# Kernel optimization log

Hardware: AMD Instinct MI355X
Metric: run time of the kernel (lower is better)

The kernel has to match this reference:

```python
import jax, jax.numpy as jnp
import numpy as np
from jax import lax

B, C_IN, C_OUT, H, W, K, MID = 16, 256, 256, 64, 64, 3, 64
BN_EPS = 1e-5


def setup_inputs() -> dict:
    key = jax.random.key(0)
    ks = jax.random.split(key, 16)
    inp = {
        'x': jax.random.normal(ks[0], (B, C_IN, H, W), dtype=jnp.float32),
        # 4 kernel banks: (4, c2, c1//g, k, k)
        'weight': jax.random.normal(ks[1], (4, C_OUT, C_IN, K, K), dtype=jnp.float32) * 0.05,
        'gamma': jnp.ones((C_OUT,), jnp.float32),
        'beta': jnp.zeros((C_OUT,), jnp.float32),
    }
    # four attention branches: Linear(c, mid, bias=False) -> ReLU -> Linear(mid, 4, bias=True)
    names = ['s', 'c', 'f', 'w']
    for i, n in enumerate(names):
        inp[f'fc_{n}_w1'] = jax.random.normal(ks[2 + 3 * i], (MID, C_IN), dtype=jnp.float32) * 0.05
        inp[f'fc_{n}_w2'] = jax.random.normal(ks[3 + 3 * i], (4, MID), dtype=jnp.float32) * 0.05
        inp[f'fc_{n}_b2'] = jax.random.normal(ks[4 + 3 * i], (4,), dtype=jnp.float32) * 0.05
    return inp


def _branch(pooled, w1, w2, b2):
    # pooled: [B, C]; w1: [MID, C]; w2: [4, MID]
    h = jax.nn.relu(pooled @ w1.T)
    return jax.nn.softmax(h @ w2.T + b2, axis=1)  # [B, 4]


def reference(x, weight, gamma, beta,
              fc_s_w1, fc_s_w2, fc_s_b2,
              fc_c_w1, fc_c_w2, fc_c_b2,
              fc_f_w1, fc_f_w2, fc_f_b2,
              fc_w_w1, fc_w_w2, fc_w_b2):
    b = x.shape[0]
    pooled = jnp.mean(x, axis=(2, 3))  # GAP -> [B, C]
    alpha = (_branch(pooled, fc_s_w1, fc_s_w2, fc_s_b2)
             * _branch(pooled, fc_c_w1, fc_c_w2, fc_c_b2)
             * _branch(pooled, fc_f_w1, fc_f_w2, fc_f_b2)
             * _branch(pooled, fc_w_w1, fc_w_w2, fc_w_b2))  # [B, 4]
    # per-sample dynamic kernels: [B, out_c, in_c, k, k]
    dyn_w = jnp.einsum('bn,noikl->boikl', alpha, weight)

    def conv_one(xi, wi):
        # xi: [C, H, W]; wi: [out_c, in_c, k, k]
        return lax.conv_general_dilated(
            xi[None], wi, window_strides=(1, 1), padding='SAME',
            dimension_numbers=('NCHW', 'OIHW', 'NCHW'))[0]

    out = jax.vmap(conv_one)(x, dyn_w)  # [B, out_c, H, W]

    # BatchNorm2d (training-mode batch statistics)
    mean = jnp.mean(out, axis=(0, 2, 3))
    var = jnp.var(out, axis=(0, 2, 3))
    out = (out - mean[None, :, None, None]) * jax.lax.rsqrt(var + BN_EPS)[None, :, None, None]
    return out * gamma[None, :, None, None] + beta[None, :, None, None]
```

## Files before the change

### kernel.cpp

```cpp
#include <hip/hip_runtime.h>
#include <math.h>

#define BB 16
#define CIN 256
#define COUT 256
#define HH 64
#define WW 64
#define NBANK_STRIDE 589824

typedef short bf16x8 __attribute__((ext_vector_type(8)));
typedef float f32x4 __attribute__((ext_vector_type(4)));

#define WS_XT_OFF 32768
#define WS_DW_OFF 33587200
#define WS_NEED   52461568ULL

static __device__ __forceinline__ short f2bf(float f) {
    union { float f; unsigned u; } v; v.f = f;
    unsigned r = v.u + 0x7FFF + ((v.u >> 16) & 1);
    return (short)(r >> 16);
}

struct AttnParams {
    const float* w1[4];
    const float* w2[4];
    const float* b2[4];
};

__global__ __launch_bounds__(256) void zero_kernel(float* __restrict__ ws) {
    ws[blockIdx.x * 256 + threadIdx.x] = 0.f;
}

__global__ __launch_bounds__(256) void xpose_kernel(const float* __restrict__ x,
                                                    short* __restrict__ xT,
                                                    float* __restrict__ pooled) {
    const int ci0 = blockIdx.x * 32;
    const int h = blockIdx.y;
    const int b = blockIdx.z;
    const int t = threadIdx.x;
    __shared__ __align__(16) short tile[64][40];
    {
        const int ci = t >> 3;
        const int l = t & 7;
        const float4* src = (const float4*)(x + ((size_t)(b * 256 + ci0 + ci)) * 4096 + h * 64);
        float4 v1 = src[l * 2];
        float4 v2 = src[l * 2 + 1];
        tile[l * 8 + 0][ci] = f2bf(v1.x);
        tile[l * 8 + 1][ci] = f2bf(v1.y);
        tile[l * 8 + 2][ci] = f2bf(v1.z);
        tile[l * 8 + 3][ci] = f2bf(v1.w);
        tile[l * 8 + 4][ci] = f2bf(v2.x);
        tile[l * 8 + 5][ci] = f2bf(v2.y);
        tile[l * 8 + 6][ci] = f2bf(v2.z);
        tile[l * 8 + 7][ci] = f2bf(v2.w);
        float s = v1.x + v1.y + v1.z + v1.w + v2.x + v2.y + v2.z + v2.w;
        s += __shfl_xor(s, 1, 64);
        s += __shfl_xor(s, 2, 64);
        s += __shfl_xor(s, 4, 64);
        if (l == 0) atomicAdd(&pooled[b * 256 + ci0 + ci], s);
    }
    __syncthreads();
    {
        const int w = t >> 2;
        const int s = t & 3;
        bf16x8 val = *(const bf16x8*)&tile[w][s * 8];
        *(bf16x8*)&xT[((size_t)b * 4096 + h * 64 + w) * 256 + ci0 + s * 8] = val;
    }
}

__global__ __launch_bounds__(256) void attn_kernel(AttnParams p, float* __restrict__ ws_f) {
    const int b = blockIdx.x;
    const int t = threadIdx.x;
    const int wv = t >> 6;
    const int lane = t & 63;
    __shared__ float ps[256];
    __shared__ float hs[4][64];
    __shared__ float lg[4][4];
    __shared__ float sm[4][4];
    ws_f[4096 + b * 256 + t] = 0.f;
    ps[t] = ws_f[b * 256 + t] * (1.0f / 4096.0f);
    __syncthreads();
    {
        const float4* w1v = (const float4*)(p.w1[wv] + lane * 256);
        float h = 0.f;
#pragma unroll 8
        for (int i = 0; i < 64; ++i) {
            float4 w4 = w1v[i];
            h += w4.x * ps[i * 4 + 0] + w4.y * ps[i * 4 + 1] +
                 w4.z * ps[i * 4 + 2] + w4.w * ps[i * 4 + 3];
        }
        hs[wv][lane] = fmaxf(h, 0.f);
    }
    __syncthreads();
    if (t < 16) {
        const int n = t >> 2, j = t & 3;
        const float* w2 = p.w2[n];
        float l = p.b2[n][j];
        for (int m = 0; m < 64; ++m) l += w2[j * 64 + m] * hs[n][m];
        lg[n][j] = l;
    }
    __syncthreads();
    if (t < 4) {
        const int n = t;
        float mx = fmaxf(fmaxf(lg[n][0], lg[n][1]), fmaxf(lg[n][2], lg[n][3]));
        float e0 = expf(lg[n][0] - mx), e1 = expf(lg[n][1] - mx);
        float e2 = expf(lg[n][2] - mx), e3 = expf(lg[n][3] - mx);
        float inv = 1.f / (e0 + e1 + e2 + e3);
        sm[n][0] = e0 * inv; sm[n][1] = e1 * inv; sm[n][2] = e2 * inv; sm[n][3] = e3 * inv;
    }
    __syncthreads();
    if (t < 4) ws_f[b * 256 + t] = sm[0][t] * sm[1][t] * sm[2][t] * sm[3][t];
}

__global__ __launch_bounds__(256) void dynw_kernel(const float* __restrict__ wt,
                                                   const float* __restrict__ ws_f,
                                                   short* __restrict__ dynwT) {
    const int co = blockIdx.x;
    const int ci = threadIdx.x;
    float w[4][9];
#pragma unroll
    for (int n = 0; n < 4; ++n) {
        const size_t base = ((size_t)(n * 256 + co) * 256 + ci) * 9;
#pragma unroll
        for (int k = 0; k < 9; ++k) w[n][k] = wt[base + k];
    }
    for (int b = 0; b < BB; ++b) {
        const float a0 = ws_f[b * 256 + 0];
        const float a1 = ws_f[b * 256 + 1];
        const float a2 = ws_f[b * 256 + 2];
        const float a3 = ws_f[b * 256 + 3];
#pragma unroll
        for (int k = 0; k < 9; ++k) {
            float v = a0 * w[0][k] + a1 * w[1][k] + a2 * w[2][k] + a3 * w[3][k];
            dynwT[((size_t)(b * 9 + k) * 256 + co) * 256 + ci] = f2bf(v);
        }
    }
}

__global__ __launch_bounds__(256, 2) void conv_mfma_kernel(const short* __restrict__ xT,
                                                           const short* __restrict__ dynwT,
                                                           float* __restrict__ out,
                                                           float* __restrict__ bn_part) {
    const int nt = blockIdx.x;
    const int mt = blockIdx.y;
    const int b = blockIdx.z;
    const int t = threadIdx.x;
    const int lane = t & 63;
    const int wv = t >> 6;
    const int wx = wv & 1;
    const int wy = wv >> 1;
    const int mh = lane & 15;
    const int q = lane >> 4;
    const int r0 = nt * 4;
    const int co0 = mt * 128;

    __shared__ __align__(16) short xs[396 * 40];
    __shared__ __align__(16) short As[2][128 * 40];
    __shared__ float red[128][2][2];

    f32x4 acc[4][8];
#pragma unroll
    for (int i = 0; i < 4; ++i)
#pragma unroll
        for (int j = 0; j < 8; ++j) acc[i][j] = (f32x4){0.f, 0.f, 0.f, 0.f};

    const int arow0 = t >> 2;
    const int asub = t & 3;
    const short* Ab = dynwT + (size_t)b * 9 * 65536 + (co0 + arow0) * 256 + asub * 8;
    const int a_lds0 = arow0 * 40 + asub * 8;
    const int a_lds1 = (arow0 + 64) * 40 + asub * 8;
    const int a_rd = (wy * 64 + mh) * 40 + q * 8;

    const bf16x8 zero8 = {0, 0, 0, 0, 0, 0, 0, 0};

    for (int cc = 0; cc < 8; ++cc) {
        const int ci0 = cc * 32;
        __syncthreads();
        bf16x8 pa0 = *(const bf16x8*)(Ab + ci0);
        bf16x8 pa1 = *(const bf16x8*)(Ab + 64 * 256 + ci0);
#pragma unroll
        for (int i = 0; i < 7; ++i) {
            int idx = t + 256 * i;
            if (idx < 1584) {
                int p = idx >> 2;
                int sub = idx & 3;
                int lr = p / 66;
                int lc = p - lr * 66;
                int r = r0 - 1 + lr;
                int c = lc - 1;
                bf16x8 v = zero8;
                if ((unsigned)r < 64u && (unsigned)c < 64u)
                    v = *(const bf16x8*)&xT[((size_t)b * 4096 + r * 64 + c) * 256 + ci0 + sub * 8];
                *(bf16x8*)&xs[p * 40 + sub * 8] = v;
            }
        }
        *(bf16x8*)&As[0][a_lds0] = pa0;
        *(bf16x8*)&As[0][a_lds1] = pa1;
        __syncthreads();
#pragma unroll
        for (int khw = 0; khw < 9; ++khw) {
            const int kh = khw / 3;
            const int kw = khw - kh * 3;
            bf16x8 na0, na1;
            if (khw < 8) {
                na0 = *(const bf16x8*)(Ab + (khw + 1) * 65536 + ci0);
                na1 = *(const bf16x8*)(Ab + (khw + 1) * 65536 + 64 * 256 + ci0);
            }
            bf16x8 bfr[8];
#pragma unroll
            for (int ni = 0; ni < 8; ++ni) {
                const int row_l = wx * 2 + (ni >> 2) + kh;
                const int col_l = (ni & 3) * 16 + kw + mh;
                bfr[ni] = *(const bf16x8*)&xs[(row_l * 66 + col_l) * 40 + q * 8];
            }
#pragma unroll
            for (int mi = 0; mi < 4; ++mi) {
                bf16x8 af = *(const bf16x8*)&As[khw & 1][a_rd + mi * 640];
#pragma unroll
                for (int ni = 0; ni < 8; ++ni)
                    acc[mi][ni] = __builtin_amdgcn_mfma_f32_16x16x32_bf16(af, bfr[ni], acc[mi][ni], 0, 0, 0);
            }
            if (khw < 8) {
                *(bf16x8*)&As[(khw + 1) & 1][a_lds0] = na0;
                *(bf16x8*)&As[(khw + 1) & 1][a_lds1] = na1;
            }
            __syncthreads();
        }
    }

    float s16[4][4], q16[4][4];
#pragma unroll
    for (int mi = 0; mi < 4; ++mi)
#pragma unroll
        for (int reg = 0; reg < 4; ++reg) { s16[mi][reg] = 0.f; q16[mi][reg] = 0.f; }

#pragma unroll
    for (int mi = 0; mi < 4; ++mi) {
#pragma unroll
        for (int ni = 0; ni < 8; ++ni) {
            const int pix = wx * 128 + ni * 16 + mh;
            const int h = r0 + (pix >> 6);
            const int w = pix & 63;
#pragma unroll
            for (int reg = 0; reg < 4; ++reg) {
                const int co = co0 + wy * 64 + mi * 16 + q * 4 + reg;
                const float e = acc[mi][ni][reg];
                out[(((size_t)b * 256 + co) << 12) + (h << 6) + w] = e;
                s16[mi][reg] += e;
                q16[mi][reg] += e * e;
            }
        }
    }
#pragma unroll
    for (int mi = 0; mi < 4; ++mi)
#pragma unroll
        for (int reg = 0; reg < 4; ++reg) {
            float s = s16[mi][reg], sq = q16[mi][reg];
            s += __shfl_xor(s, 1, 64);  sq += __shfl_xor(sq, 1, 64);
            s += __shfl_xor(s, 2, 64);  sq += __shfl_xor(sq, 2, 64);
            s += __shfl_xor(s, 4, 64);  sq += __shfl_xor(sq, 4, 64);
            s += __shfl_xor(s, 8, 64);  sq += __shfl_xor(sq, 8, 64);
            if (mh == 0) {
                const int co_l = wy * 64 + mi * 16 + q * 4 + reg;
                red[co_l][0][wx] = s;
                red[co_l][1][wx] = sq;
            }
        }
    __syncthreads();
    {
        const int co_l = t >> 1;
        const int st = t & 1;
        float v = red[co_l][st][0] + red[co_l][st][1];
        atomicAdd(&bn_part[(st * 256 + co0 + co_l) * 8 + (nt & 7)], v);
    }
}

__global__ __launch_bounds__(256) void bn_finalize_kernel(const float* __restrict__ bn_part,
                                                          const float* __restrict__ gamma,
                                                          const float* __restrict__ beta,
                                                          float* __restrict__ scale,
                                                          float* __restrict__ shift) {
    const int co = threadIdx.x;
    float S = 0.f, Q = 0.f;
#pragma unroll
    for (int s = 0; s < 8; ++s) {
        S += bn_part[(co) * 8 + s];
        Q += bn_part[(256 + co) * 8 + s];
    }
    const float mean = S * (1.f / 65536.f);
    const float var = Q * (1.f / 65536.f) - mean * mean;
    const float inv = rsqrtf(var + 1e-5f);
    const float sc = gamma[co] * inv;
    scale[co] = sc;
    shift[co] = beta[co] - mean * sc;
}

__global__ __launch_bounds__(256) void bn_apply_kernel(float* __restrict__ out,
                                                       const float* __restrict__ scale,
                                                       const float* __restrict__ shift) {
    const int gid = blockIdx.x * 256 + threadIdx.x;
    const int c = (gid >> 10) & 255;
    float4* p = (float4*)out;
    float4 v = p[gid];
    const float sc = scale[c], sh = shift[c];
    v.x = v.x * sc + sh;
    v.y = v.y * sc + sh;
    v.z = v.z * sc + sh;
    v.w = v.w * sc + sh;
    p[gid] = v;
}

__global__ __launch_bounds__(256) void gap_kernel(const float* __restrict__ x,
                                                  float* __restrict__ pooled) {
    const int plane = blockIdx.x;
    const float4* p = (const float4*)(x + (size_t)plane * 4096);
    const int t = threadIdx.x;
    float s = 0.f;
#pragma unroll
    for (int i = 0; i < 4; ++i) {
        float4 v = p[t + 256 * i];
        s += v.x + v.y + v.z + v.w;
    }
#pragma unroll
    for (int off = 32; off > 0; off >>= 1) s += __shfl_down(s, off, 64);
    __shared__ float red[4];
    if ((t & 63) == 0) red[t >> 6] = s;
    __syncthreads();
    if (t == 0) pooled[plane] = (red[0] + red[1] + red[2] + red[3]) * (1.0f / 4096.0f);
}

__global__ __launch_bounds__(64) void attn64_kernel(const float* __restrict__ pooled,
                                                    AttnParams p,
                                                    float* __restrict__ alpha) {
    const int b = blockIdx.x;
    const int t = threadIdx.x;
    __shared__ float ps[256];
    __shared__ float hs[64];
    __shared__ float lg[4];
    __shared__ float prod[4];
#pragma unroll
    for (int i = 0; i < 4; ++i) ps[t + 64 * i] = pooled[b * 256 + t + 64 * i];
    if (t < 4) prod[t] = 1.f;
    __syncthreads();
    for (int n = 0; n < 4; ++n) {
        const float* w1 = p.w1[n];
        float h = 0.f;
        for (int c = 0; c < 256; ++c) h += w1[t * 256 + c] * ps[c];
        hs[t] = fmaxf(h, 0.f);
        __syncthreads();
        if (t < 4) {
            const float* w2 = p.w2[n];
            float l = p.b2[n][t];
            for (int m = 0; m < 64; ++m) l += w2[t * 64 + m] * hs[m];
            lg[t] = l;
        }
        __syncthreads();
        if (t == 0) {
            float mx = fmaxf(fmaxf(lg[0], lg[1]), fmaxf(lg[2], lg[3]));
            float e0 = expf(lg[0] - mx), e1 = expf(lg[1] - mx);
            float e2 = expf(lg[2] - mx), e3 = expf(lg[3] - mx);
            float inv = 1.f / (e0 + e1 + e2 + e3);
            prod[0] *= e0 * inv; prod[1] *= e1 * inv;
            prod[2] *= e2 * inv; prod[3] *= e3 * inv;
        }
        __syncthreads();
    }
    if (t < 4) alpha[b * 4 + t] = prod[t];
}

__global__ __launch_bounds__(256) void conv_fp32_kernel(const float* __restrict__ x,
                                                        const float* __restrict__ wt,
                                                        const float* __restrict__ alpha,
                                                        float* __restrict__ out) {
    const int h = blockIdx.x;
    const int cot = blockIdx.y;
    const int b = blockIdx.z;
    const int t = threadIdx.x;
    const int tx = t & 15;
    const int ty = t >> 4;
    const int co0 = cot * 64;
    __shared__ __align__(16) float xsf[32][68];
    __shared__ __align__(16) float wshf[3][32][68];
    const float a0 = alpha[b * 4 + 0], a1 = alpha[b * 4 + 1];
    const float a2 = alpha[b * 4 + 2], a3 = alpha[b * 4 + 3];
    float acc[4][4];
#pragma unroll
    for (int i = 0; i < 4; ++i)
#pragma unroll
        for (int j = 0; j < 4; ++j) acc[i][j] = 0.f;
    const size_t xbase = (size_t)b * CIN * 4096;
    for (int kh = 0; kh < 3; ++kh) {
        const int r = h + kh - 1;
        if (r < 0 || r >= HH) continue;
        for (int chunk = 0; chunk < 8; ++chunk) {
            const int ci0 = chunk * 32;
            __syncthreads();
#pragma unroll
            for (int i = 0; i < 8; ++i) {
                int flat = t + 256 * i;
                int ci = flat >> 6;
                int w = flat & 63;
                xsf[ci][1 + w] = x[xbase + (size_t)(ci0 + ci) * 4096 + r * 64 + w];
            }
            if (t < 32) { xsf[t][0] = 0.f; xsf[t][65] = 0.f; xsf[t][66] = 0.f; xsf[t][67] = 0.f; }
#pragma unroll
            for (int j = 0; j < 24; ++j) {
                int e = t + 256 * j;
                int co = e / 96;
                int rem = e - co * 96;
                int ci = rem / 3;
                int kw = rem - ci * 3;
                size_t g = (((size_t)(co0 + co) * 256 + (ci0 + ci)) * 3 + kh) * 3 + kw;
                wshf[kw][ci][co] = a0 * wt[g] + a1 * wt[g + NBANK_STRIDE] +
                                   a2 * wt[g + 2 * NBANK_STRIDE] + a3 * wt[g + 3 * NBANK_STRIDE];
            }
            __syncthreads();
            for (int ci = 0; ci < 32; ++ci) {
                float4 w0 = *(const float4*)&wshf[0][ci][tx * 4];
                float4 w1v = *(const float4*)&wshf[1][ci][tx * 4];
                float4 w2v = *(const float4*)&wshf[2][ci][tx * 4];
                float4 xa = *(const float4*)&xsf[ci][ty * 4];
                float4 xb = *(const float4*)&xsf[ci][ty * 4 + 4];
                float v[8] = {xa.x, xa.y, xa.z, xa.w, xb.x, xb.y, xb.z, xb.w};
                float aw[3][4] = {{w0.x, w0.y, w0.z, w0.w},
                                  {w1v.x, w1v.y, w1v.z, w1v.w},
                                  {w2v.x, w2v.y, w2v.z, w2v.w}};
#pragma unroll
                for (int kw = 0; kw < 3; ++kw)
#pragma unroll
                    for (int i = 0; i < 4; ++i)
#pragma unroll
                        for (int j = 0; j < 4; ++j)
                            acc[i][j] += aw[kw][i] * v[j + kw];
            }
        }
    }
    size_t obase = (((size_t)b * COUT + co0 + tx * 4) * 64 + h) * 64 + ty * 4;
#pragma unroll
    for (int i = 0; i < 4; ++i) {
        float4 o = {acc[i][0], acc[i][1], acc[i][2], acc[i][3]};
        *(float4*)&out[obase + (size_t)i * 4096] = o;
    }
}

__global__ __launch_bounds__(256) void bn_stats_kernel(const float* __restrict__ out,
                                                       const float* __restrict__ gamma,
                                                       const float* __restrict__ beta,
                                                       float* __restrict__ scale,
                                                       float* __restrict__ shift) {
    const int co = blockIdx.x;
    const int t = threadIdx.x;
    float s = 0.f, sq = 0.f;
    for (int b = 0; b < BB; ++b) {
        const float4* p = (const float4*)(out + ((size_t)b * 256 + co) * 4096);
#pragma unroll
        for (int i = 0; i < 4; ++i) {
            float4 v = p[t + 256 * i];
            s += v.x + v.y + v.z + v.w;
            sq += v.x * v.x + v.y * v.y + v.z * v.z + v.w * v.w;
        }
    }
#pragma unroll
    for (int off = 32; off > 0; off >>= 1) {
        s += __shfl_down(s, off, 64);
        sq += __shfl_down(sq, off, 64);
    }
    __shared__ float rs[4], rq[4];
    if ((t & 63) == 0) { rs[t >> 6] = s; rq[t >> 6] = sq; }
    __syncthreads();
    if (t == 0) {
        float S = rs[0] + rs[1] + rs[2] + rs[3];
        float Q = rq[0] + rq[1] + rq[2] + rq[3];
        float mean = S * (1.f / 65536.f);
        float var = Q * (1.f / 65536.f) - mean * mean;
        float inv = rsqrtf(var + 1e-5f);
        float sc = gamma[co] * inv;
        scale[co] = sc;
        shift[co] = beta[co] - mean * sc;
    }
}

extern "C" void kernel_launch(void* const* d_in, const int* in_sizes, int n_in,
                              void* d_out, int out_size, void* d_ws, size_t ws_size,
                              hipStream_t stream) {
    (void)in_sizes; (void)n_in; (void)out_size;
    const float* x = (const float*)d_in[0];
    const float* wt = (const float*)d_in[1];
    const float* gamma = (const float*)d_in[2];
    const float* beta = (const float*)d_in[3];
    AttnParams ap;
    for (int n = 0; n < 4; ++n) {
        ap.w1[n] = (const float*)d_in[4 + 3 * n];
        ap.w2[n] = (const float*)d_in[5 + 3 * n];
        ap.b2[n] = (const float*)d_in[6 + 3 * n];
    }
    float* ws_f = (float*)d_ws;
    float* out = (float*)d_out;

    if (ws_size >= WS_NEED) {
        short* xT = (short*)((char*)d_ws + WS_XT_OFF);
        short* dynwT = (short*)((char*)d_ws + WS_DW_OFF);
        float* bn_part = ws_f + 4096;
        float* scale = ws_f;
        float* shift = ws_f + 256;

        zero_kernel<<<16, 256, 0, stream>>>(ws_f);
        xpose_kernel<<<dim3(8, 64, 16), 256, 0, stream>>>(x, xT, ws_f);
        attn_kernel<<<16, 256, 0, stream>>>(ap, ws_f);
        dynw_kernel<<<256, 256, 0, stream>>>(wt, ws_f, dynwT);
        conv_mfma_kernel<<<dim3(16, 2, 16), 256, 0, stream>>>(xT, dynwT, out, bn_part);
        bn_finalize_kernel<<<1, 256, 0, stream>>>(bn_part, gamma, beta, scale, shift);
        bn_apply_kernel<<<16384, 256, 0, stream>>>(out, scale, shift);
    } else {
        float* pooled = ws_f;
        float* alpha = ws_f + 4096;
        float* scale = ws_f + 4160;
        float* shift = ws_f + 4416;
        gap_kernel<<<4096, 256, 0, stream>>>(x, pooled);
        attn64_kernel<<<16, 64, 0, stream>>>(pooled, ap, alpha);
        conv_fp32_kernel<<<dim3(64, 4, 16), 256, 0, stream>>>(x, wt, alpha, out);
        bn_stats_kernel<<<256, 256, 0, stream>>>(out, gamma, beta, scale, shift);
        bn_apply_kernel<<<16384, 256, 0, stream>>>(out, scale, shift);
    }
}
```

Before: 277.8 us.

## Load conv weight fragments directly to registers, fold BN finalize into apply, stage dynw via LDS

The conv kernel no longer stages the dynamic-weight A tile in shared memory. Each lane loads its MFMA A fragments straight from global memory into registers, prefetched one k-step ahead across channel chunks, which removes the per-khw __syncthreads and LDS writes and reads. The BN finalize kernel is merged into the apply kernel, so each block recomputes its channel's scale and shift, saving one launch. dynw_kernel now loads the weights coalesced into LDS before the per-thread gather. The trade-off is more global-memory traffic for the A operand, since each wave loads its own fragments, plus higher register pressure.

```diff
diff --git a/kernel.cpp b/kernel.cpp
--- a/kernel.cpp
+++ b/kernel.cpp
@@ -116,14 +116,21 @@
                                                    const float* __restrict__ ws_f,
                                                    short* __restrict__ dynwT) {
     const int co = blockIdx.x;
-    const int ci = threadIdx.x;
+    const int t = threadIdx.x;
+    __shared__ float wl[4][2304];
+#pragma unroll
+    for (int n = 0; n < 4; ++n) {
+        const float* src = wt + ((size_t)(n * 256 + co)) * 2304;
+#pragma unroll
+        for (int i = 0; i < 9; ++i) wl[n][t + 256 * i] = src[t + 256 * i];
+    }
+    __syncthreads();
+    const int ci = t;
     float w[4][9];
 #pragma unroll
-    for (int n = 0; n < 4; ++n) {
-        const size_t base = ((size_t)(n * 256 + co) * 256 + ci) * 9;
-#pragma unroll
-        for (int k = 0; k < 9; ++k) w[n][k] = wt[base + k];
-    }
+    for (int n = 0; n < 4; ++n)
+#pragma unroll
+        for (int k = 0; k < 9; ++k) w[n][k] = wl[n][ci * 9 + k];
     for (int b = 0; b < BB; ++b) {
         const float a0 = ws_f[b * 256 + 0];
         const float a1 = ws_f[b * 256 + 1];
@@ -155,7 +162,6 @@
     const int co0 = mt * 128;
 
     __shared__ __align__(16) short xs[396 * 40];
-    __shared__ __align__(16) short As[2][128 * 40];
     __shared__ float red[128][2][2];
 
     f32x4 acc[4][8];
@@ -164,20 +170,17 @@
 #pragma unroll
         for (int j = 0; j < 8; ++j) acc[i][j] = (f32x4){0.f, 0.f, 0.f, 0.f};
 
-    const int arow0 = t >> 2;
-    const int asub = t & 3;
-    const short* Ab = dynwT + (size_t)b * 9 * 65536 + (co0 + arow0) * 256 + asub * 8;
-    const int a_lds0 = arow0 * 40 + asub * 8;
-    const int a_lds1 = (arow0 + 64) * 40 + asub * 8;
-    const int a_rd = (wy * 64 + mh) * 40 + q * 8;
+    const short* Abase = dynwT + (size_t)b * 9 * 65536 + (size_t)(co0 + wy * 64 + mh) * 256 + q * 8;
+
+    bf16x8 ca[4], na[4];
+#pragma unroll
+    for (int mi = 0; mi < 4; ++mi) ca[mi] = *(const bf16x8*)(Abase + mi * 4096);
 
     const bf16x8 zero8 = {0, 0, 0, 0, 0, 0, 0, 0};
 
     for (int cc = 0; cc < 8; ++cc) {
         const int ci0 = cc * 32;
         __syncthreads();
-        bf16x8 pa0 = *(const bf16x8*)(Ab + ci0);
-        bf16x8 pa1 = *(const bf16x8*)(Ab + 64 * 256 + ci0);
 #pragma unroll
         for (int i = 0; i < 7; ++i) {
             int idx = t + 256 * i;
@@ -194,18 +197,18 @@
                 *(bf16x8*)&xs[p * 40 + sub * 8] = v;
             }
         }
-        *(bf16x8*)&As[0][a_lds0] = pa0;
-        *(bf16x8*)&As[0][a_lds1] = pa1;
         __syncthreads();
 #pragma unroll
         for (int khw = 0; khw < 9; ++khw) {
+            const int kk = cc * 9 + khw;
+            const int nk = (kk < 71) ? kk + 1 : 71;
+            const int nkhw = nk - (nk / 9) * 9;
+            const int nci0 = (nk / 9) * 32;
+#pragma unroll
+            for (int mi = 0; mi < 4; ++mi)
+                na[mi] = *(const bf16x8*)(Abase + (size_t)nkhw * 65536 + mi * 4096 + nci0);
             const int kh = khw / 3;
             const int kw = khw - kh * 3;
-            bf16x8 na0, na1;
-            if (khw < 8) {
-                na0 = *(const bf16x8*)(Ab + (khw + 1) * 65536 + ci0);
-                na1 = *(const bf16x8*)(Ab + (khw + 1) * 65536 + 64 * 256 + ci0);
-            }
             bf16x8 bfr[8];
 #pragma unroll
             for (int ni = 0; ni < 8; ++ni) {
@@ -214,17 +217,12 @@
                 bfr[ni] = *(const bf16x8*)&xs[(row_l * 66 + col_l) * 40 + q * 8];
             }
 #pragma unroll
-            for (int mi = 0; mi < 4; ++mi) {
-                bf16x8 af = *(const bf16x8*)&As[khw & 1][a_rd + mi * 640];
+            for (int mi = 0; mi < 4; ++mi)
 #pragma unroll
                 for (int ni = 0; ni < 8; ++ni)
-                    acc[mi][ni] = __builtin_amdgcn_mfma_f32_16x16x32_bf16(af, bfr[ni], acc[mi][ni], 0, 0, 0);
-            }
-            if (khw < 8) {
-                *(bf16x8*)&As[(khw + 1) & 1][a_lds0] = na0;
-                *(bf16x8*)&As[(khw + 1) & 1][a_lds1] = na1;
-            }
-            __syncthreads();
+                    acc[mi][ni] = __builtin_amdgcn_mfma_f32_16x16x32_bf16(ca[mi], bfr[ni], acc[mi][ni], 0, 0, 0);
+#pragma unroll
+            for (int mi = 0; mi < 4; ++mi) ca[mi] = na[mi];
         }
     }
 
@@ -275,34 +273,31 @@
     }
 }
 
-__global__ __launch_bounds__(256) void bn_finalize_kernel(const float* __restrict__ bn_part,
-                                                          const float* __restrict__ gamma,
-                                                          const float* __restrict__ beta,
-                                                          float* __restrict__ scale,
-                                                          float* __restrict__ shift) {
-    const int co = threadIdx.x;
-    float S = 0.f, Q = 0.f;
-#pragma unroll
-    for (int s = 0; s < 8; ++s) {
-        S += bn_part[(co) * 8 + s];
-        Q += bn_part[(256 + co) * 8 + s];
-    }
-    const float mean = S * (1.f / 65536.f);
-    const float var = Q * (1.f / 65536.f) - mean * mean;
-    const float inv = rsqrtf(var + 1e-5f);
-    const float sc = gamma[co] * inv;
-    scale[co] = sc;
-    shift[co] = beta[co] - mean * sc;
-}
-
 __global__ __launch_bounds__(256) void bn_apply_kernel(float* __restrict__ out,
-                                                       const float* __restrict__ scale,
-                                                       const float* __restrict__ shift) {
+                                                       const float* __restrict__ bn_part,
+                                                       const float* __restrict__ gamma,
+                                                       const float* __restrict__ beta) {
     const int gid = blockIdx.x * 256 + threadIdx.x;
-    const int c = (gid >> 10) & 255;
+    const int c = (blockIdx.x >> 2) & 255;
+    __shared__ float ssc, ssh;
+    if (threadIdx.x == 0) {
+        float S = 0.f, Q = 0.f;
+#pragma unroll
+        for (int s = 0; s < 8; ++s) {
+            S += bn_part[c * 8 + s];
+            Q += bn_part[(256 + c) * 8 + s];
+        }
+        const float mean = S * (1.f / 65536.f);
+        const float var = Q * (1.f / 65536.f) - mean * mean;
+        const float inv = rsqrtf(var + 1e-5f);
+        const float sc = gamma[c] * inv;
+        ssc = sc;
+        ssh = beta[c] - mean * sc;
+    }
+    __syncthreads();
     float4* p = (float4*)out;
     float4 v = p[gid];
-    const float sc = scale[c], sh = shift[c];
+    const float sc = ssc, sh = ssh;
     v.x = v.x * sc + sh;
     v.y = v.y * sc + sh;
     v.z = v.z * sc + sh;
@@ -478,6 +473,21 @@
         scale[co] = sc;
         shift[co] = beta[co] - mean * sc;
     }
+}
+
+__global__ __launch_bounds__(256) void bn_apply_old_kernel(float* __restrict__ out,
+                                                           const float* __restrict__ scale,
+                                                           const float* __restrict__ shift) {
+    const int gid = blockIdx.x * 256 + threadIdx.x;
+    const int c = (gid >> 10) & 255;
+    float4* p = (float4*)out;
+    float4 v = p[gid];
+    const float sc = scale[c], sh = shift[c];
+    v.x = v.x * sc + sh;
+    v.y = v.y * sc + sh;
+    v.z = v.z * sc + sh;
+    v.w = v.w * sc + sh;
+    p[gid] = v;
 }
 
 extern "C" void kernel_launch(void* const* d_in, const int* in_sizes, int n_in,
@@ -501,16 +511,13 @@
         short* xT = (short*)((char*)d_ws + WS_XT_OFF);
         short* dynwT = (short*)((char*)d_ws + WS_DW_OFF);
         float* bn_part = ws_f + 4096;
-        float* scale = ws_f;
-        float* shift = ws_f + 256;
 
         zero_kernel<<<16, 256, 0, stream>>>(ws_f);
         xpose_kernel<<<dim3(8, 64, 16), 256, 0, stream>>>(x, xT, ws_f);
         attn_kernel<<<16, 256, 0, stream>>>(ap, ws_f);
         dynw_kernel<<<256, 256, 0, stream>>>(wt, ws_f, dynwT);
         conv_mfma_kernel<<<dim3(16, 2, 16), 256, 0, stream>>>(xT, dynwT, out, bn_part);
-        bn_finalize_kernel<<<1, 256, 0, stream>>>(bn_part, gamma, beta, scale, shift);
-        bn_apply_kernel<<<16384, 256, 0, stream>>>(out, scale, shift);
+        bn_apply_kernel<<<16384, 256, 0, stream>>>(out, bn_part, gamma, beta);
     } else {
         float* pooled = ws_f;
         float* alpha = ws_f + 4096;
@@ -520,6 +527,6 @@
         attn64_kernel<<<16, 64, 0, stream>>>(pooled, ap, alpha);
         conv_fp32_kernel<<<dim3(64, 4, 16), 256, 0, stream>>>(x, wt, alpha, out);
         bn_stats_kernel<<<256, 256, 0, stream>>>(out, gamma, beta, scale, shift);
-        bn_apply_kernel<<<16384, 256, 0, stream>>>(out, scale, shift);
-    }
-}
+        bn_apply_old_kernel<<<16384, 256, 0, stream>>>(out, scale, shift);
+    }
+}
```

Measured after the change: 382.3 us. 1.38x slower.
